# Kernel tuning notes

Measured on AMD Instinct MI355X. Metric: run time of the kernel, lower is better.

The kernel has to match this reference:

```python
import jax, jax.numpy as jnp
import numpy as np

LAM = 0.1   # smooth_param
EPS = 1e-8  # torch cosine_similarity eps


def setup_inputs() -> dict:
    key = jax.random.key(0)
    k1, k2, k3 = jax.random.split(key, 3)
    B, num_supp, num_query, T, D = 8, 5, 128, 16, 2048
    supp = jax.random.normal(k1, (B, num_supp, T, D), jnp.float32)
    query = jax.random.normal(k2, (B, num_query, T, D), jnp.float32)
    query_ys = jax.random.randint(k3, (B * num_query,), 0, num_supp)
    return {"supp": supp, "query": query, "query_ys": query_ys}


def _cosine_dist(supp, query):
    # supp: (B, ns, T, D), query: (B, nq, T, D)
    # dist[b,q,s,l,m] = 1 - cos(supp[b,s,l], query[b,q,m]); batch order (b,q,s)
    B, ns, T, D = supp.shape
    nq = query.shape[1]
    dots = jnp.einsum('bsld,bqmd->bqslm', supp, query)
    sn = jnp.linalg.norm(supp, axis=-1)   # (B, ns, T)
    qn = jnp.linalg.norm(query, axis=-1)  # (B, nq, T)
    denom = jnp.maximum(sn[:, None, :, :, None] * qn[:, :, None, None, :], EPS)
    dist = 1.0 - dots / denom
    return dist.reshape(B * nq * ns, T, T)


def _dtw(dist):
    # Relaxed (soft-min) OTAM band DP. dist: (N, T, T) -> (N,)
    # opt grid is (T, T+2) with zero-padded columns m=0 and m=T+1.
    N, T, _ = dist.shape
    dist_pad = jnp.pad(dist, ((0, 0), (0, 0), (1, 1)))  # (N, T, T+2)
    # Row l=0: opt[0,m] = cumsum of dist_pad[0, :m+1]
    row0 = jnp.cumsum(dist_pad[:, 0, :], axis=-1)  # (N, T+2)

    m_idx = jnp.arange(1, T + 2)
    boundary = (m_idx == 1) | (m_idx == T + 1)  # 3-way softmin only at band edges

    def row_step(prev_row, dist_row):
        # prev_row: (N, T+2) = opt[l-1]; dist_row: (N, T+2) = dist_pad[:, l]
        def col_step(left, xs):
            diag, up, d, is_b = xs  # each (N,) except is_b scalar bool
            s2 = jnp.logaddexp(-diag / LAM, -left / LAM)        # {diag, left}
            s3 = jnp.logaddexp(s2, -up / LAM)                   # + {up}
            val = -LAM * jnp.where(is_b, s3, s2) + d
            return val, val

        xs = (prev_row[:, :-1].T, prev_row[:, 1:].T, dist_row[:, 1:].T, boundary)
        init = jnp.zeros((N,), dist_row.dtype)  # opt[l, 0] = 0
        _, cols = jax.lax.scan(col_step, init, xs)  # (T+1, N)
        new_row = jnp.concatenate([init[:, None], cols.T], axis=1)  # (N, T+2)
        return new_row, None

    rows = jnp.swapaxes(dist_pad[:, 1:, :], 0, 1)  # (T-1, N, T+2)
    final_row, _ = jax.lax.scan(row_step, row0, rows)
    return final_row[:, -1]  # opt[:, T-1, T+1]


def _cross_entropy(logits, labels):
    logp = jax.nn.log_softmax(logits, axis=-1)
    return -jnp.mean(jnp.take_along_axis(logp, labels[:, None], axis=1))


def reference(supp, query, query_ys):
    ns = supp.shape[1]
    dist = _cosine_dist(supp, query)            # (B*nq*ns, T, T)
    tam1 = _dtw(dist).reshape(-1, ns)           # forward-direction alignment
    tam2 = _dtw(dist[:, ::-1, ::-1]).reshape(-1, ns)  # flipped (dims 1,2)
    loss1 = _cross_entropy(-tam1, query_ys)
    loss2 = _cross_entropy(-tam2, query_ys)
    loss = 0.5 * (loss1 + loss2)
    tam = 0.5 * (tam1 + tam2)
    return loss, tam
```

## Files before the change

### kernel.cpp

```cpp
#include <hip/hip_runtime.h>
#include <hip/hip_bf16.h>

#define NB   8
#define NS   5
#define NQ   128
#define TT   16
#define DD   2048
#define NROW 1024
#define NSROW (NB * NS * TT)
#define KQ   512
#define LDQ  520
#define LAMI 10.0f
#define LAMF 0.1f

typedef __attribute__((ext_vector_type(8))) short  short8;
typedef __attribute__((ext_vector_type(4))) float  float4v;

static __device__ __forceinline__ unsigned int cvtpk(float x, float y) {
    unsigned int r;
    asm("v_cvt_pk_bf16_f32 %0, %1, %2" : "=v"(r) : "v"(x), "v"(y));
    return r;
}

static __device__ __forceinline__ float dpp_shr1(float x) {
    int r = __builtin_amdgcn_update_dpp(0, __builtin_bit_cast(int, x),
                                        0x138 , 0xF, 0xF, true);
    return __builtin_bit_cast(float, r);
}

__global__ __launch_bounds__(256) void
preproc_supp(const float* __restrict__ supp, unsigned short* __restrict__ suppBf,
             float* __restrict__ suppSq, float* __restrict__ loss0)
{
    if (blockIdx.x == 0 && threadIdx.x == 0) loss0[0] = 0.f;
    const int wave = threadIdx.x >> 6, lane = threadIdx.x & 63;
    const int row = blockIdx.x * 4 + wave;
    const float* src = supp + (size_t)row * DD;
    unsigned short* dst = suppBf + (size_t)row * DD;
    float ss = 0.f;
    #pragma unroll
    for (int i = 0; i < 8; ++i) {
        float4 v = *reinterpret_cast<const float4*>(src + i * 256 + lane * 4);
        uint2 pv = { cvtpk(v.x, v.y), cvtpk(v.z, v.w) };
        *reinterpret_cast<uint2*>(dst + i * 256 + lane * 4) = pv;
        ss += v.x * v.x + v.y * v.y + v.z * v.z + v.w * v.w;
    }
    #pragma unroll
    for (int off = 32; off >= 1; off >>= 1) ss += __shfl_xor(ss, off, 64);
    if (lane == 0) suppSq[row] = ss;
}

__global__ __launch_bounds__(512, 8) void
dist_dtw_kernel(const unsigned short* __restrict__ suppBf, const float* __restrict__ suppSq,
                const float* __restrict__ query, const int* __restrict__ ys,
                float* __restrict__ out)
{
    __shared__ __align__(16) unsigned short sB[2][TT * LDQ];
    __shared__ float ssq[96];
    __shared__ float distS[NS][TT][TT];
    __shared__ float tamv[16];

    const int tid  = threadIdx.x;
    const int blk  = blockIdx.x;
    const int wave = tid >> 6;
    const int lane = tid & 63;
    const int fr   = lane & 15;
    const int quad = lane >> 4;

    const int qr = tid >> 5;
    const int qc = tid & 31;
    const float* qsrc = query + (size_t)(blk * TT + qr) * DD;

    float ss = 0.f;

    {
        float4 v[4];
        #pragma unroll
        for (int i = 0; i < 4; ++i)
            v[i] = *reinterpret_cast<const float4*>(qsrc + 4 * (qc + i * 32));
        #pragma unroll
        for (int i = 0; i < 4; ++i) {
            uint2 pv = { cvtpk(v[i].x, v[i].y), cvtpk(v[i].z, v[i].w) };
            *reinterpret_cast<uint2*>(&sB[0][qr * LDQ + 4 * (qc + i * 32)]) = pv;
            ss += v[i].x * v[i].x + v[i].y * v[i].y + v[i].z * v[i].z + v[i].w * v[i].w;
        }
        if (tid < 80) ssq[tid] = suppSq[(blk >> 7) * (NS * TT) + tid];
    }
    __syncthreads();

    float4v acc0 = {0.f, 0.f, 0.f, 0.f}, acc1 = {0.f, 0.f, 0.f, 0.f};
    const unsigned short* ap =
        suppBf + ((size_t)((blk >> 7) * NS + wave) * TT + fr) * DD + quad * 8;

    #pragma unroll
    for (int p = 0; p < 4; ++p) {
        float4 v[4];
        if (p < 3) {
            #pragma unroll
            for (int i = 0; i < 4; ++i)
                v[i] = *reinterpret_cast<const float4*>(
                    qsrc + (p + 1) * KQ + 4 * (qc + i * 32));
        }
        if (wave < NS) {
            const unsigned short* a = ap + p * KQ;
            const unsigned short* b = &sB[p & 1][fr * LDQ + quad * 8];
            #pragma unroll
            for (int k = 0; k < 16; k += 2) {
                short8 a0 = *reinterpret_cast<const short8*>(a + k * 32);
                short8 a1 = *reinterpret_cast<const short8*>(a + k * 32 + 32);
                short8 b0 = *reinterpret_cast<const short8*>(b + k * 32);
                short8 b1 = *reinterpret_cast<const short8*>(b + k * 32 + 32);
                acc0 = __builtin_amdgcn_mfma_f32_16x16x32_bf16(a0, b0, acc0, 0, 0, 0);
                acc1 = __builtin_amdgcn_mfma_f32_16x16x32_bf16(a1, b1, acc1, 0, 0, 0);
            }
        }
        if (p < 3) {
            #pragma unroll
            for (int i = 0; i < 4; ++i) {
                uint2 pv = { cvtpk(v[i].x, v[i].y), cvtpk(v[i].z, v[i].w) };
                *reinterpret_cast<uint2*>(&sB[(p + 1) & 1][qr * LDQ + 4 * (qc + i * 32)]) = pv;
                ss += v[i].x * v[i].x + v[i].y * v[i].y + v[i].z * v[i].z + v[i].w * v[i].w;
            }
            __syncthreads();
        }
    }

    #pragma unroll
    for (int off = 16; off >= 1; off >>= 1) ss += __shfl_xor(ss, off, 32);
    if (qc == 0) ssq[80 + qr] = ss;
    __syncthreads();

    if (wave < NS) {
        float qn = sqrtf(ssq[80 + fr]);
        #pragma unroll
        for (int r = 0; r < 4; ++r) {
            int l = quad * 4 + r;
            float denom = fmaxf(sqrtf(ssq[wave * 16 + l]) * qn, 1e-8f);
            distS[wave][l][fr] = 1.0f - (acc0[r] + acc1[r]) / denom;
        }
    }
    __syncthreads();

    if (wave < NS && (lane & 31) <= 17) {
        const int g    = lane & 31;
        const int dir  = lane >> 5;
        const int s    = wave;
        const bool isb = (g == 1) | (g == 17);
        float val = 0.f, vprev = 0.f;
        #pragma unroll
        for (int t = 1; t <= 32; ++t) {
            float left = dpp_shr1(val);
            float diag = dpp_shr1(vprev);
            int l = t - g;
            if (g >= 1 && l >= 0 && l <= 15) {
                float d = 0.f;
                if (g <= 16) d = dir ? distS[s][15 - l][16 - g] : distS[s][l][g - 1];
                float nv;
                if (l == 0) {
                    nv = left + d;
                } else {
                    float am = -LAMI * diag, bm = -LAMI * left;
                    float mx = fmaxf(am, bm);
                    float s3 = 0.f;
                    if (isb) {
                        float cm = -LAMI * val;
                        float m3 = fmaxf(mx, cm);
                        s3 = __expf(cm - m3);
                        mx = m3;
                    }
                    float ssum = __expf(am - mx) + __expf(bm - mx) + s3;
                    nv = fmaf(-LAMF, mx + __logf(ssum), d);
                }
                vprev = val; val = nv;
            }
        }
        if (g == 17) tamv[s * 2 + dir] = val;
    }
    __syncthreads();

    if (tid < NS) {
        out[1 + blk * NS + tid] = 0.5f * (tamv[2 * tid] + tamv[2 * tid + 1]);
    }
    if (tid == 0) {
        float t1v[NS], t2v[NS];
        #pragma unroll
        for (int s = 0; s < NS; ++s) { t1v[s] = tamv[2 * s]; t2v[s] = tamv[2 * s + 1]; }
        const int y = ys[blk];

        float mx1 = -t1v[0], mx2 = -t2v[0];
        #pragma unroll
        for (int s = 1; s < NS; ++s) { mx1 = fmaxf(mx1, -t1v[s]); mx2 = fmaxf(mx2, -t2v[s]); }
        float s1 = 0.f, s2 = 0.f;
        #pragma unroll
        for (int s = 0; s < NS; ++s) { s1 += __expf(-t1v[s] - mx1); s2 += __expf(-t2v[s] - mx2); }
        float lse1  = mx1 + __logf(s1);
        float lse2v = mx2 + __logf(s2);

        float ty1 = t1v[0], ty2 = t2v[0];
        #pragma unroll
        for (int s = 1; s < NS; ++s) { if (y == s) { ty1 = t1v[s]; ty2 = t2v[s]; } }

        float c = 0.5f * ((lse1 + ty1) + (lse2v + ty2));
        atomicAdd(out, c * (1.0f / (float)NROW));
    }
}

extern "C" void kernel_launch(void* const* d_in, const int* in_sizes, int n_in,
                              void* d_out, int out_size, void* d_ws, size_t ws_size,
                              hipStream_t stream) {
    const float* supp  = (const float*)d_in[0];
    const float* query = (const float*)d_in[1];
    const int*   ys    = (const int*)d_in[2];
    float* out = (float*)d_out;

    float* suppSq = (float*)d_ws;
    unsigned short* suppBf = (unsigned short*)(suppSq + NSROW);

    preproc_supp<<<NSROW / 4, 256, 0, stream>>>(supp, suppBf, suppSq, out);
    dist_dtw_kernel<<<NROW, 512, 0, stream>>>(suppBf, suppSq, query, ys, out);
}
```

Measured before the change: 245.1 us.

## Split K across waves with direct-register query loads and LDS reduction

Replaces the 512-thread block, which staged bf16 query tiles in LDS with double buffering and gave each support to its own wave, with a 256-thread block. Each of the four waves takes a quarter of D, loads query fragments straight from global memory into MFMA operands, and computes all five supports. Partial accumulators are then summed through LDS. The DTW lanes are repacked three chains per wave to fit the smaller block. This drops the LDS staging and the per-phase barriers, and the wave that held no support, in exchange for a cross-wave reduction and less regular global query access.

```diff
diff --git a/kernel.cpp b/kernel.cpp
--- a/kernel.cpp
+++ b/kernel.cpp
@@ -8,8 +8,7 @@
 #define DD   2048
 #define NROW 1024
 #define NSROW (NB * NS * TT)
-#define KQ   512
-#define LDQ  520
+#define KSL  512
 #define LAMI 10.0f
 #define LAMF 0.1f
 
@@ -50,15 +49,17 @@
     if (lane == 0) suppSq[row] = ss;
 }
 
-__global__ __launch_bounds__(512, 8) void
-dist_dtw_kernel(const unsigned short* __restrict__ suppBf, const float* __restrict__ suppSq,
-                const float* __restrict__ query, const int* __restrict__ ys,
-                float* __restrict__ out)
+__global__ __launch_bounds__(256, 4) void
+dist_dtw_wave(const unsigned short* __restrict__ suppBf, const float* __restrict__ suppSq,
+              const float* __restrict__ query, const int* __restrict__ ys,
+              float* __restrict__ out)
 {
-    __shared__ __align__(16) unsigned short sB[2][TT * LDQ];
-    __shared__ float ssq[96];
+    __shared__ __align__(16) float red[4][NS][64][4];
+    __shared__ float qsqp[4][16];
+    __shared__ float qq[16];
     __shared__ float distS[NS][TT][TT];
-    __shared__ float tamv[16];
+    __shared__ float ssqS[80];
+    __shared__ float tamv[12];
 
     const int tid  = threadIdx.x;
     const int blk  = blockIdx.x;
@@ -67,126 +68,113 @@
     const int fr   = lane & 15;
     const int quad = lane >> 4;
 
-    const int qr = tid >> 5;
-    const int qc = tid & 31;
-    const float* qsrc = query + (size_t)(blk * TT + qr) * DD;
-
+    if (tid < 80) ssqS[tid] = suppSq[(blk >> 7) * (NS * TT) + tid];
+
+    const float* qp = query + (size_t)(blk * TT + fr) * DD + wave * KSL + quad * 8;
+    const unsigned short* aps[NS];
+    #pragma unroll
+    for (int s = 0; s < NS; ++s)
+        aps[s] = suppBf + ((size_t)((blk >> 7) * NS + s) * TT + fr) * DD
+               + wave * KSL + quad * 8;
+
+    float4v acc[NS];
+    #pragma unroll
+    for (int s = 0; s < NS; ++s) acc[s] = (float4v){0.f, 0.f, 0.f, 0.f};
     float ss = 0.f;
 
+    #pragma unroll 2
+    for (int kk = 0; kk < 16; ++kk) {
+        float4 q0 = *reinterpret_cast<const float4*>(qp + kk * 32);
+        float4 q1 = *reinterpret_cast<const float4*>(qp + kk * 32 + 4);
+        union { unsigned int u[4]; short8 v; } qu;
+        qu.u[0] = cvtpk(q0.x, q0.y); qu.u[1] = cvtpk(q0.z, q0.w);
+        qu.u[2] = cvtpk(q1.x, q1.y); qu.u[3] = cvtpk(q1.z, q1.w);
+        ss += q0.x*q0.x + q0.y*q0.y + q0.z*q0.z + q0.w*q0.w
+            + q1.x*q1.x + q1.y*q1.y + q1.z*q1.z + q1.w*q1.w;
+        #pragma unroll
+        for (int s = 0; s < NS; ++s) {
+            short8 a = *reinterpret_cast<const short8*>(aps[s] + kk * 32);
+            acc[s] = __builtin_amdgcn_mfma_f32_16x16x32_bf16(a, qu.v, acc[s], 0, 0, 0);
+        }
+    }
+
+    ss += __shfl_xor(ss, 16, 64);
+    ss += __shfl_xor(ss, 32, 64);
+    if (lane < 16) qsqp[wave][lane] = ss;
+    #pragma unroll
+    for (int s = 0; s < NS; ++s)
+        *reinterpret_cast<float4v*>(red[wave][s][lane]) = acc[s];
+    __syncthreads();
+
+    if (tid < 16) qq[tid] = qsqp[0][tid] + qsqp[1][tid] + qsqp[2][tid] + qsqp[3][tid];
+    __syncthreads();
+
+    for (int p = tid; p < NS * 64; p += 256) {
+        int t = p >> 6, ln = p & 63;
+        float4v s4 = *reinterpret_cast<const float4v*>(red[0][t][ln]);
+        #pragma unroll
+        for (int w = 1; w < 4; ++w) {
+            float4v r = *reinterpret_cast<const float4v*>(red[w][t][ln]);
+            s4[0] += r[0]; s4[1] += r[1]; s4[2] += r[2]; s4[3] += r[3];
+        }
+        int m = ln & 15, qd = ln >> 4;
+        float qn = sqrtf(qq[m]);
+        #pragma unroll
+        for (int r = 0; r < 4; ++r) {
+            int l = qd * 4 + r;
+            float denom = fmaxf(sqrtf(ssqS[t * 16 + l]) * qn, 1e-8f);
+            distS[t][l][m] = 1.0f - s4[r] / denom;
+        }
+    }
+    __syncthreads();
+
     {
-        float4 v[4];
-        #pragma unroll
-        for (int i = 0; i < 4; ++i)
-            v[i] = *reinterpret_cast<const float4*>(qsrc + 4 * (qc + i * 32));
-        #pragma unroll
-        for (int i = 0; i < 4; ++i) {
-            uint2 pv = { cvtpk(v[i].x, v[i].y), cvtpk(v[i].z, v[i].w) };
-            *reinterpret_cast<uint2*>(&sB[0][qr * LDQ + 4 * (qc + i * 32)]) = pv;
-            ss += v[i].x * v[i].x + v[i].y * v[i].y + v[i].z * v[i].z + v[i].w * v[i].w;
-        }
-        if (tid < 80) ssq[tid] = suppSq[(blk >> 7) * (NS * TT) + tid];
-    }
-    __syncthreads();
-
-    float4v acc0 = {0.f, 0.f, 0.f, 0.f}, acc1 = {0.f, 0.f, 0.f, 0.f};
-    const unsigned short* ap =
-        suppBf + ((size_t)((blk >> 7) * NS + wave) * TT + fr) * DD + quad * 8;
-
-    #pragma unroll
-    for (int p = 0; p < 4; ++p) {
-        float4 v[4];
-        if (p < 3) {
+        const int grp  = lane / 21;
+        const int g    = lane - grp * 21;
+        const int slot = wave * 3 + grp;
+        float val = 0.f, vprev = 0.f;
+        if (grp < 3 && slot < 10 && g <= 17) {
+            const int s    = slot >> 1;
+            const int dir  = slot & 1;
+            const bool isb = (g == 1) | (g == 17);
             #pragma unroll
-            for (int i = 0; i < 4; ++i)
-                v[i] = *reinterpret_cast<const float4*>(
-                    qsrc + (p + 1) * KQ + 4 * (qc + i * 32));
-        }
-        if (wave < NS) {
-            const unsigned short* a = ap + p * KQ;
-            const unsigned short* b = &sB[p & 1][fr * LDQ + quad * 8];
-            #pragma unroll
-            for (int k = 0; k < 16; k += 2) {
-                short8 a0 = *reinterpret_cast<const short8*>(a + k * 32);
-                short8 a1 = *reinterpret_cast<const short8*>(a + k * 32 + 32);
-                short8 b0 = *reinterpret_cast<const short8*>(b + k * 32);
-                short8 b1 = *reinterpret_cast<const short8*>(b + k * 32 + 32);
-                acc0 = __builtin_amdgcn_mfma_f32_16x16x32_bf16(a0, b0, acc0, 0, 0, 0);
-                acc1 = __builtin_amdgcn_mfma_f32_16x16x32_bf16(a1, b1, acc1, 0, 0, 0);
+            for (int t = 1; t <= 32; ++t) {
+                float left = dpp_shr1(val);
+                float diag = dpp_shr1(vprev);
+                int l = t - g;
+                if (g >= 1 && l >= 0 && l <= 15) {
+                    float d = 0.f;
+                    if (g <= 16) d = dir ? distS[s][15 - l][16 - g] : distS[s][l][g - 1];
+                    float nv;
+                    if (l == 0) {
+                        nv = left + d;
+                    } else {
+                        float am = -LAMI * diag, bm = -LAMI * left;
+                        float mx = fmaxf(am, bm);
+                        float s3 = 0.f;
+                        if (isb) {
+                            float cm = -LAMI * val;
+                            float m3 = fmaxf(mx, cm);
+                            s3 = __expf(cm - m3);
+                            mx = m3;
+                        }
+                        float ssum = __expf(am - mx) + __expf(bm - mx) + s3;
+                        nv = fmaf(-LAMF, mx + __logf(ssum), d);
+                    }
+                    vprev = val; val = nv;
+                }
             }
-        }
-        if (p < 3) {
-            #pragma unroll
-            for (int i = 0; i < 4; ++i) {
-                uint2 pv = { cvtpk(v[i].x, v[i].y), cvtpk(v[i].z, v[i].w) };
-                *reinterpret_cast<uint2*>(&sB[(p + 1) & 1][qr * LDQ + 4 * (qc + i * 32)]) = pv;
-                ss += v[i].x * v[i].x + v[i].y * v[i].y + v[i].z * v[i].z + v[i].w * v[i].w;
-            }
-            __syncthreads();
-        }
-    }
-
-    #pragma unroll
-    for (int off = 16; off >= 1; off >>= 1) ss += __shfl_xor(ss, off, 32);
-    if (qc == 0) ssq[80 + qr] = ss;
-    __syncthreads();
-
-    if (wave < NS) {
-        float qn = sqrtf(ssq[80 + fr]);
-        #pragma unroll
-        for (int r = 0; r < 4; ++r) {
-            int l = quad * 4 + r;
-            float denom = fmaxf(sqrtf(ssq[wave * 16 + l]) * qn, 1e-8f);
-            distS[wave][l][fr] = 1.0f - (acc0[r] + acc1[r]) / denom;
-        }
-    }
-    __syncthreads();
-
-    if (wave < NS && (lane & 31) <= 17) {
-        const int g    = lane & 31;
-        const int dir  = lane >> 5;
-        const int s    = wave;
-        const bool isb = (g == 1) | (g == 17);
-        float val = 0.f, vprev = 0.f;
-        #pragma unroll
-        for (int t = 1; t <= 32; ++t) {
-            float left = dpp_shr1(val);
-            float diag = dpp_shr1(vprev);
-            int l = t - g;
-            if (g >= 1 && l >= 0 && l <= 15) {
-                float d = 0.f;
-                if (g <= 16) d = dir ? distS[s][15 - l][16 - g] : distS[s][l][g - 1];
-                float nv;
-                if (l == 0) {
-                    nv = left + d;
-                } else {
-                    float am = -LAMI * diag, bm = -LAMI * left;
-                    float mx = fmaxf(am, bm);
-                    float s3 = 0.f;
-                    if (isb) {
-                        float cm = -LAMI * val;
-                        float m3 = fmaxf(mx, cm);
-                        s3 = __expf(cm - m3);
-                        mx = m3;
-                    }
-                    float ssum = __expf(am - mx) + __expf(bm - mx) + s3;
-                    nv = fmaf(-LAMF, mx + __logf(ssum), d);
-                }
-                vprev = val; val = nv;
-            }
-        }
-        if (g == 17) tamv[s * 2 + dir] = val;
-    }
-    __syncthreads();
-
-    if (tid < NS) {
-        out[1 + blk * NS + tid] = 0.5f * (tamv[2 * tid] + tamv[2 * tid + 1]);
-    }
+            if (g == 17) tamv[slot] = val;
+        }
+    }
+    __syncthreads();
+
+    if (tid < NS) out[1 + blk * NS + tid] = 0.5f * (tamv[2 * tid] + tamv[2 * tid + 1]);
     if (tid == 0) {
         float t1v[NS], t2v[NS];
         #pragma unroll
         for (int s = 0; s < NS; ++s) { t1v[s] = tamv[2 * s]; t2v[s] = tamv[2 * s + 1]; }
         const int y = ys[blk];
-
         float mx1 = -t1v[0], mx2 = -t2v[0];
         #pragma unroll
         for (int s = 1; s < NS; ++s) { mx1 = fmaxf(mx1, -t1v[s]); mx2 = fmaxf(mx2, -t2v[s]); }
@@ -195,11 +183,9 @@
         for (int s = 0; s < NS; ++s) { s1 += __expf(-t1v[s] - mx1); s2 += __expf(-t2v[s] - mx2); }
         float lse1  = mx1 + __logf(s1);
         float lse2v = mx2 + __logf(s2);
-
         float ty1 = t1v[0], ty2 = t2v[0];
         #pragma unroll
         for (int s = 1; s < NS; ++s) { if (y == s) { ty1 = t1v[s]; ty2 = t2v[s]; } }
-
         float c = 0.5f * ((lse1 + ty1) + (lse2v + ty2));
         atomicAdd(out, c * (1.0f / (float)NROW));
     }
@@ -217,5 +203,5 @@
     unsigned short* suppBf = (unsigned short*)(suppSq + NSROW);
 
     preproc_supp<<<NSROW / 4, 256, 0, stream>>>(supp, suppBf, suppSq, out);
-    dist_dtw_kernel<<<NROW, 512, 0, stream>>>(suppBf, suppSq, query, ys, out);
-}
+    dist_dtw_wave<<<NROW, 256, 0, stream>>>(suppBf, suppSq, query, ys, out);
+}
```

Measured after the change: 229.8 us. 1.07x faster.
